# Kernel tuning notes

Measured on AMD Instinct MI355X. Metric: run time of the kernel, lower is better.

Reference implementation:

```python
import jax, jax.numpy as jnp
import numpy as np


def setup_inputs() -> dict:
    key = jax.random.key(0)
    k1, k2, k3, k4 = jax.random.split(key, 4)
    B, C, H, W = 2, 3, 160, 160
    n, L, s, k = 3000, 72, 4, 5
    return {
        "x": jax.random.normal(k1, (B, C, H, W), dtype=jnp.float32),
        "queries": jax.random.normal(k2, (B, L, H, W), dtype=jnp.float32),
        "keys": jax.random.normal(k3, (n, L), dtype=jnp.float32),
        "values": jax.random.normal(k4, (n, s * s, k * k), dtype=jnp.float32),
        "s": s,
        "k": k,
    }


def reference(x, queries, keys, values, s, k):
    B, C, H, W = x.shape
    pad = k // 2
    # reflect-pad spatial dims (matches F.pad mode='reflect')
    xp = jnp.pad(x, ((0, 0), (0, 0), (pad, pad), (pad, pad)), mode="reflect")
    # extract k*k patches: [B, C, H, W, k*k] (fixed small loop over k*k offsets)
    patches = jnp.stack(
        [xp[:, :, i : i + H, j : j + W] for i in range(k) for j in range(k)],
        axis=-1,
    )
    # per-pixel top-1 routing over codebook keys
    q = queries.transpose(0, 2, 3, 1)  # [B, H, W, L]
    sim = jnp.einsum("bhwl,nl->bhwn", q, keys)  # [B, H, W, n]
    idx = jnp.argmax(sim, axis=-1)  # [B, H, W] int
    v = values[idx]  # gather per-pixel kernel: [B, H, W, s^2, k^2]
    # per-pixel dynamic conv: [B, C, s^2, H, W]
    out = jnp.einsum("bchwk,bhwsk->bcshw", patches, v)
    # pixel shuffle with upscale s: [B, C, s^2, H, W] -> [B, C, H*s, W*s]
    out = out.reshape(B, C, s, s, H, W)
    out = out.transpose(0, 1, 4, 2, 5, 3)  # [B, C, H, s, W, s]
    return out.reshape(B, C, H * s, W * s)
```

## Files before the change

### kernel.cpp

```cpp
#include <hip/hip_runtime.h>

#define H 160
#define W 160
#define HW 25600
#define BB 2
#define CC 3
#define LL 72
#define NKEYS 3000
#define NT 94
#define NSPL 4
#define NPIX (BB * HW)

#define CERR 3e-5f
#define ABSG 1e-3f

typedef __attribute__((ext_vector_type(8))) short bf8v;
typedef __attribute__((ext_vector_type(16))) float f16v;

union FU { uint4 u4; bf8v v; };

#define WS_KFRAG 1024
#define WS_B1    963584
#define WS_B2    1782784
#define WS_BI    2601984
#define WS_THR   3421184
#define WS_LIST  3625984
#define WS_IDX   3830784

__device__ inline unsigned bf16rn(float f) {
    unsigned u = __float_as_uint(f);
    return (u + 0x7FFFu + ((u >> 16) & 1u)) >> 16;
}

__global__ __launch_bounds__(64) void kprep_kernel(
    const float* __restrict__ keys, unsigned* __restrict__ ctrl,
    uint4* __restrict__ kfg)
{
    const int tile = blockIdx.x;
    const int lane = threadIdx.x;
    const int key  = tile * 32 + (lane & 31);
    const int half = lane >> 5;
    const bool kv  = (key < NKEYS);
    float kmax = 0.f;
#pragma unroll
    for (int ks = 0; ks < 5; ++ks) {
        unsigned wh[4], wl[4];
#pragma unroll
        for (int j = 0; j < 4; ++j) {
            const int l0 = ks * 16 + half * 8 + 2 * j;
            float v0 = (kv && l0     < LL) ? keys[(size_t)key * LL + l0]     : 0.f;
            float v1 = (kv && l0 + 1 < LL) ? keys[(size_t)key * LL + l0 + 1] : 0.f;
            kmax = fmaxf(kmax, fmaxf(fabsf(v0), fabsf(v1)));
            unsigned h0 = bf16rn(v0), h1 = bf16rn(v1);
            float r0 = v0 - __uint_as_float(h0 << 16);
            float r1 = v1 - __uint_as_float(h1 << 16);
            wh[j] = h0 | (h1 << 16);
            wl[j] = bf16rn(r0) | (bf16rn(r1) << 16);
        }
        const int base = tile * 640 + (ks * 2) * 64 + lane;
        kfg[base]      = make_uint4(wh[0], wh[1], wh[2], wh[3]);
        kfg[base + 64] = make_uint4(wl[0], wl[1], wl[2], wl[3]);
    }
#pragma unroll
    for (int m = 32; m >= 1; m >>= 1)
        kmax = fmaxf(kmax, __shfl_xor(kmax, m));
    if (lane == 0) atomicMax(&ctrl[1], __float_as_uint(kmax));
}

__device__ __forceinline__ void build_qfrag(
    const float* __restrict__ qp, int hv, FU* qh, FU* ql, float& Ssum)
{
    Ssum = 0.f;
#pragma unroll
    for (int ks = 0; ks < 5; ++ks) {
        unsigned wh[4], wl[4];
#pragma unroll
        for (int j = 0; j < 4; ++j) {
            const int l0 = ks * 16 + hv * 8 + 2 * j;
            float v0 = (l0     < LL) ? qp[(size_t)l0 * HW]       : 0.f;
            float v1 = (l0 + 1 < LL) ? qp[(size_t)(l0 + 1) * HW] : 0.f;
            Ssum += fabsf(v0) + fabsf(v1);
            unsigned h0 = bf16rn(v0), h1 = bf16rn(v1);
            float r0 = v0 - __uint_as_float(h0 << 16);
            float r1 = v1 - __uint_as_float(h1 << 16);
            wh[j] = h0 | (h1 << 16);
            wl[j] = bf16rn(r0) | (bf16rn(r1) << 16);
        }
        qh[ks].u4 = make_uint4(wh[0], wh[1], wh[2], wh[3]);
        ql[ks].u4 = make_uint4(wl[0], wl[1], wl[2], wl[3]);
    }
}

template<bool LAST>
__device__ __forceinline__ void do_tile2(
    const uint4* __restrict__ kfg, int tileIdx,
    const FU* __restrict__ qhA, const FU* __restrict__ qlA,
    const FU* __restrict__ qhB, const FU* __restrict__ qlB,
    int lane, int hb,
    float& b1A, float& b2A, int& biA,
    float& b1B, float& b2B, int& biB)
{
    const uint4* __restrict__ kt = kfg + (size_t)tileIdx * 640;
    f16v accA, accB;
#pragma unroll
    for (int r = 0; r < 16; ++r) { accA[r] = 0.f; accB[r] = 0.f; }
#pragma unroll
    for (int ks = 0; ks < 5; ++ks) {
        FU kh, kl;
        kh.u4 = kt[ks * 128 + lane];
        kl.u4 = kt[ks * 128 + 64 + lane];
        accA = __builtin_amdgcn_mfma_f32_32x32x16_bf16(kh.v, qhA[ks].v, accA, 0, 0, 0);
        accB = __builtin_amdgcn_mfma_f32_32x32x16_bf16(kh.v, qhB[ks].v, accB, 0, 0, 0);
        accA = __builtin_amdgcn_mfma_f32_32x32x16_bf16(kh.v, qlA[ks].v, accA, 0, 0, 0);
        accB = __builtin_amdgcn_mfma_f32_32x32x16_bf16(kh.v, qlB[ks].v, accB, 0, 0, 0);
        accA = __builtin_amdgcn_mfma_f32_32x32x16_bf16(kl.v, qhA[ks].v, accA, 0, 0, 0);
        accB = __builtin_amdgcn_mfma_f32_32x32x16_bf16(kl.v, qhB[ks].v, accB, 0, 0, 0);
    }
    const int kb0 = tileIdx * 32 + hb;
    const int NR = LAST ? 12 : 16;
#pragma unroll
    for (int r = 0; r < NR; ++r) {
        const int key = kb0 + ((r & 3) + 8 * (r >> 2));
        {
            const float s = accA[r];
            const float n2 = __builtin_amdgcn_fmed3f(b1A, b2A, s);
            const bool gt = (s > b1A);
            b1A = fmaxf(b1A, s); b2A = n2; biA = gt ? key : biA;
        }
        {
            const float s = accB[r];
            const float n2 = __builtin_amdgcn_fmed3f(b1B, b2B, s);
            const bool gt = (s > b1B);
            b1B = fmaxf(b1B, s); b2B = n2; biB = gt ? key : biB;
        }
    }
}

__global__ __launch_bounds__(256) void route_kernel(
    const float* __restrict__ queries,
    const uint4* __restrict__ kfg,
    const unsigned* __restrict__ ctrl,
    float* __restrict__ b1s, float* __restrict__ b2s,
    int* __restrict__ bis, float* __restrict__ thr)
{
    const int tid   = threadIdx.x;
    const int lane  = tid & 63;
    const int wid   = tid >> 6;
    const int hv    = lane >> 5;
    const int hb    = 4 * hv;
    const int split = blockIdx.y;
    const int pA = blockIdx.x * 256 + wid * 64 + (lane & 31);
    const int pB = pA + 32;

    FU qhA[5], qlA[5], qhB[5], qlB[5];
    float SsA, SsB;
    {
        const int bA = pA / HW, hwA = pA - bA * HW;
        build_qfrag(queries + (size_t)bA * LL * HW + hwA, hv, qhA, qlA, SsA);
        const int bB = pB / HW, hwB = pB - bB * HW;
        build_qfrag(queries + (size_t)bB * LL * HW + hwB, hv, qhB, qlB, SsB);
    }

    float b1A = -3.0e38f, b2A = -3.0e38f; int biA = 0;
    float b1B = -3.0e38f, b2B = -3.0e38f; int biB = 0;

    const int t0 = split * 24;
    int tend = (split == NSPL - 1) ? NT : (t0 + 24);
    const bool haslast = (tend == NT);
    if (haslast) tend -= 1;

    for (int t = t0; t < tend; ++t)
        do_tile2<false>(kfg, t, qhA, qlA, qhB, qlB, lane, hb,
                        b1A, b2A, biA, b1B, b2B, biB);
    if (haslast)
        do_tile2<true >(kfg, NT - 1, qhA, qlA, qhB, qlB, lane, hb,
                        b1A, b2A, biA, b1B, b2B, biB);

    const float o1A = __shfl_xor(b1A, 32), o2A = __shfl_xor(b2A, 32);
    const int   oiA = __shfl_xor(biA, 32);
    const float n2A = fmaxf(fminf(b1A, o1A), fmaxf(b2A, o2A));
    const bool  tkA = (o1A > b1A) || (o1A == b1A && oiA < biA);
    const float n1A = fmaxf(b1A, o1A);
    const int   niA = tkA ? oiA : biA;

    const float o1B = __shfl_xor(b1B, 32), o2B = __shfl_xor(b2B, 32);
    const int   oiB = __shfl_xor(biB, 32);
    const float n2B = fmaxf(fminf(b1B, o1B), fmaxf(b2B, o2B));
    const bool  tkB = (o1B > b1B) || (o1B == b1B && oiB < biB);
    const float n1B = fmaxf(b1B, o1B);
    const int   niB = tkB ? oiB : biB;

    if ((lane & 32) == 0) {
        const int sp = split * NPIX;
        b1s[sp + pA] = n1A; b2s[sp + pA] = n2A; bis[sp + pA] = niA;
        b1s[sp + pB] = n1B; b2s[sp + pB] = n2B; bis[sp + pB] = niB;
        if (split == 0) {
            const float kmax = __uint_as_float(ctrl[1]);
            const float SpA = SsA + __shfl_xor(SsA, 32);
            const float SpB = SsB + __shfl_xor(SsB, 32);
            thr[pA] = 2.0f * (CERR * SpA * kmax + ABSG);
            thr[pB] = 2.0f * (CERR * SpB * kmax + ABSG);
        }
    }
}

__global__ __launch_bounds__(256) void combine_kernel(
    const float* __restrict__ b1s, const float* __restrict__ b2s,
    const int* __restrict__ bis, const float* __restrict__ thr,
    unsigned* __restrict__ ctrl, unsigned* __restrict__ list,
    int* __restrict__ idx_buf)
{
    const int p = blockIdx.x * 256 + threadIdx.x;
    float m1 = -3.0e38f, m2 = -3.0e38f; int bi = 0;
#pragma unroll
    for (int s = 0; s < NSPL; ++s) {
        const float a1 = b1s[s * NPIX + p];
        const float a2 = b2s[s * NPIX + p];
        const int   ai = bis[s * NPIX + p];
        if (a1 > m1) { m2 = fmaxf(m1, a2); m1 = a1; bi = ai; }
        else         { m2 = fmaxf(m2, a1); }
    }
    if ((m1 - m2) > thr[p]) idx_buf[p] = bi;
    else { unsigned pos = atomicAdd(&ctrl[0], 1u); list[pos] = (unsigned)p; }
}

__global__ __launch_bounds__(256) void cleanup_kernel(
    const float* __restrict__ queries, const float* __restrict__ keys,
    const unsigned* __restrict__ ctrl, const unsigned* __restrict__ list,
    int* __restrict__ idx_buf)
{
    __shared__ float qs[LL];
    __shared__ float rbest[4];
    __shared__ int   ridx[4];

    const int tid = threadIdx.x;
    const int ln  = tid & 63;
    const int wid = tid >> 6;
    const unsigned count = ctrl[0];

    for (unsigned u = blockIdx.x; u < count; u += gridDim.x) {
        const int p  = (int)list[u];
        const int b  = p / HW;
        const int hw = p - b * HW;

        __syncthreads();
        if (tid < LL)
            qs[tid] = queries[((size_t)b * LL + tid) * HW + hw];
        __syncthreads();

        float q[LL];
#pragma unroll
        for (int l = 0; l < LL; ++l) q[l] = qs[l];

        float best = -3.0e38f; int bidx = 0x7FFFFFFF;
#pragma unroll 1
        for (int it = 0; it < 12; ++it) {
            const int n  = it * 256 + tid;
            const int nc = (n < NKEYS) ? n : (NKEYS - 1);
            const float4* __restrict__ kr = (const float4*)(keys + (size_t)nc * LL);
            float a0 = 0.f, a1 = 0.f, a2 = 0.f, a3 = 0.f;
#pragma unroll
            for (int j = 0; j < 18; ++j) {
                float4 kv = kr[j];
                a0 = fmaf(q[4 * j + 0], kv.x, a0);
                a1 = fmaf(q[4 * j + 1], kv.y, a1);
                a2 = fmaf(q[4 * j + 2], kv.z, a2);
                a3 = fmaf(q[4 * j + 3], kv.w, a3);
            }
            const float s = (a0 + a1) + (a2 + a3);
            if (n < NKEYS && (s > best || (s == best && n < bidx))) { best = s; bidx = n; }
        }
#pragma unroll
        for (int m = 32; m >= 1; m >>= 1) {
            const float ob = __shfl_xor(best, m);
            const int   oi = __shfl_xor(bidx, m);
            if (ob > best || (ob == best && oi < bidx)) { best = ob; bidx = oi; }
        }
        if (ln == 0) { rbest[wid] = best; ridx[wid] = bidx; }
        __syncthreads();
        if (tid == 0) {
            float fb = rbest[0]; int fi = ridx[0];
#pragma unroll
            for (int wvi = 1; wvi < 4; ++wvi) {
                if (rbest[wvi] > fb || (rbest[wvi] == fb && ridx[wvi] < fi)) {
                    fb = rbest[wvi]; fi = ridx[wvi];
                }
            }
            idx_buf[p] = fi;
        }
    }
}

__global__ __launch_bounds__(256) void conv_kernel(
    const float* __restrict__ x,
    const float* __restrict__ values,
    const int* __restrict__ idx_buf,
    float* __restrict__ out)
{
    const int p  = blockIdx.x * 256 + threadIdx.x;
    const int b  = p / HW;
    const int hw = p - b * HW;
    const int h  = hw / W;
    const int w  = hw - h * W;

    const int idx = idx_buf[p];

    float patch[CC][25];
#pragma unroll
    for (int i = 0; i < 5; ++i) {
        int r = h + i - 2;
        r = (r < 0) ? -r : ((r >= H) ? (2 * H - 2 - r) : r);
#pragma unroll
        for (int j = 0; j < 5; ++j) {
            int cidx = w + j - 2;
            cidx = (cidx < 0) ? -cidx : ((cidx >= W) ? (2 * W - 2 - cidx) : cidx);
#pragma unroll
            for (int c = 0; c < CC; ++c)
                patch[c][i * 5 + j] = x[((size_t)(b * CC + c) * H + r) * W + cidx];
        }
    }

    const float* vbase = values + (size_t)idx * 400;
    float acc[CC][16];
#pragma unroll
    for (int c = 0; c < CC; ++c)
#pragma unroll
        for (int si = 0; si < 16; ++si) acc[c][si] = 0.f;

#pragma unroll
    for (int si = 0; si < 16; ++si) {
        float v[25];
#pragma unroll
        for (int kk = 0; kk < 25; ++kk) v[kk] = vbase[si * 25 + kk];
#pragma unroll
        for (int c = 0; c < CC; ++c) {
            float a = 0.f;
#pragma unroll
            for (int kk = 0; kk < 25; ++kk) a += patch[c][kk] * v[kk];
            acc[c][si] = a;
        }
    }

#pragma unroll
    for (int c = 0; c < CC; ++c) {
#pragma unroll
        for (int sy = 0; sy < 4; ++sy) {
            float4 o = make_float4(acc[c][sy * 4 + 0], acc[c][sy * 4 + 1],
                                   acc[c][sy * 4 + 2], acc[c][sy * 4 + 3]);
            size_t off = ((size_t)(b * CC + c) * (H * 4) + (h * 4 + sy)) * (size_t)(W * 4)
                         + (size_t)w * 4;
            *(float4*)(&out[off]) = o;
        }
    }
}

extern "C" void kernel_launch(void* const* d_in, const int* in_sizes, int n_in,
                              void* d_out, int out_size, void* d_ws, size_t ws_size,
                              hipStream_t stream) {
    const float* x       = (const float*)d_in[0];
    const float* queries = (const float*)d_in[1];
    const float* keys    = (const float*)d_in[2];
    const float* values  = (const float*)d_in[3];
    float* out = (float*)d_out;

    char* ws = (char*)d_ws;
    unsigned* ctrl = (unsigned*)ws;
    uint4*    kfg  = (uint4*)(ws + WS_KFRAG);
    float*    b1s  = (float*)(ws + WS_B1);
    float*    b2s  = (float*)(ws + WS_B2);
    int*      bis  = (int*)(ws + WS_BI);
    float*    thr  = (float*)(ws + WS_THR);
    unsigned* list = (unsigned*)(ws + WS_LIST);
    int*      idxb = (int*)(ws + WS_IDX);

    hipMemsetAsync(d_ws, 0, 8, stream);
    kprep_kernel<<<NT, 64, 0, stream>>>(keys, ctrl, kfg);
    route_kernel<<<dim3(NPIX / 256, NSPL), 256, 0, stream>>>(queries, kfg, ctrl,
                                                             b1s, b2s, bis, thr);
    combine_kernel<<<NPIX / 256, 256, 0, stream>>>(b1s, b2s, bis, thr, ctrl, list, idxb);
    cleanup_kernel<<<2048, 256, 0, stream>>>(queries, keys, ctrl, list, idxb);
    conv_kernel<<<NPIX / 256, 256, 0, stream>>>(x, values, idxb, out);
}
```

Baseline: 167.0 us.

## Stage key tiles in LDS and process two pixel groups per wave

The routing kernel now copies each split's key fragment tiles into shared memory in two halves and has each wave process two 64-pixel groups against them, with larger 512-thread blocks and a smaller grid. The goal is to cut repeated global/L2 reads of the key fragments by reusing them across more pixels per block. In exchange, query fragments are rebuilt for each half, doubling query loads, and the large LDS footprint plus a 200-block grid reduces occupancy and CU coverage.

```diff
diff --git a/kernel.cpp b/kernel.cpp
--- a/kernel.cpp
+++ b/kernel.cpp
@@ -92,23 +92,22 @@
 }
 
 template<bool LAST>
-__device__ __forceinline__ void do_tile2(
-    const uint4* __restrict__ kfg, int tileIdx,
+__device__ __forceinline__ void comp_tile_lds(
+    const uint4* __restrict__ kb, int tileIdx,
     const FU* __restrict__ qhA, const FU* __restrict__ qlA,
     const FU* __restrict__ qhB, const FU* __restrict__ qlB,
     int lane, int hb,
     float& b1A, float& b2A, int& biA,
     float& b1B, float& b2B, int& biB)
 {
-    const uint4* __restrict__ kt = kfg + (size_t)tileIdx * 640;
     f16v accA, accB;
 #pragma unroll
     for (int r = 0; r < 16; ++r) { accA[r] = 0.f; accB[r] = 0.f; }
 #pragma unroll
     for (int ks = 0; ks < 5; ++ks) {
         FU kh, kl;
-        kh.u4 = kt[ks * 128 + lane];
-        kl.u4 = kt[ks * 128 + 64 + lane];
+        kh.u4 = kb[ks * 128 + lane];
+        kl.u4 = kb[ks * 128 + 64 + lane];
         accA = __builtin_amdgcn_mfma_f32_32x32x16_bf16(kh.v, qhA[ks].v, accA, 0, 0, 0);
         accB = __builtin_amdgcn_mfma_f32_32x32x16_bf16(kh.v, qhB[ks].v, accB, 0, 0, 0);
         accA = __builtin_amdgcn_mfma_f32_32x32x16_bf16(kh.v, qlA[ks].v, accA, 0, 0, 0);
@@ -136,70 +135,114 @@
     }
 }
 
-__global__ __launch_bounds__(256) void route_kernel(
+__device__ __forceinline__ void run_round(
+    const uint4* __restrict__ kbuf, int gtile0, int hcount, bool haslast,
+    const float* __restrict__ queries, int pA, int hv, int hb, int lane,
+    float& b1A, float& b2A, int& biA,
+    float& b1B, float& b2B, int& biB,
+    float& SsA, float& SsB)
+{
+    const int pB = pA + 32;
+    FU qhA[5], qlA[5], qhB[5], qlB[5];
+    {
+        const int bA = pA / HW, hwA = pA - bA * HW;
+        build_qfrag(queries + (size_t)bA * LL * HW + hwA, hv, qhA, qlA, SsA);
+        const int bB = pB / HW, hwB = pB - bB * HW;
+        build_qfrag(queries + (size_t)bB * LL * HW + hwB, hv, qhB, qlB, SsB);
+    }
+    const int nmain = hcount - (haslast ? 1 : 0);
+#pragma unroll 1
+    for (int t = 0; t < nmain; ++t)
+        comp_tile_lds<false>(kbuf + t * 640, gtile0 + t, qhA, qlA, qhB, qlB,
+                             lane, hb, b1A, b2A, biA, b1B, b2B, biB);
+    if (haslast)
+        comp_tile_lds<true>(kbuf + (hcount - 1) * 640, gtile0 + hcount - 1,
+                            qhA, qlA, qhB, qlB, lane, hb,
+                            b1A, b2A, biA, b1B, b2B, biB);
+}
+
+__global__ __launch_bounds__(512, 2) void route_kernel(
     const float* __restrict__ queries,
     const uint4* __restrict__ kfg,
     const unsigned* __restrict__ ctrl,
     float* __restrict__ b1s, float* __restrict__ b2s,
     int* __restrict__ bis, float* __restrict__ thr)
 {
+    __shared__ uint4 kbuf[12 * 640];
+
     const int tid   = threadIdx.x;
     const int lane  = tid & 63;
     const int wid   = tid >> 6;
     const int hv    = lane >> 5;
     const int hb    = 4 * hv;
     const int split = blockIdx.y;
-    const int pA = blockIdx.x * 256 + wid * 64 + (lane & 31);
-    const int pB = pA + 32;
-
-    FU qhA[5], qlA[5], qhB[5], qlB[5];
-    float SsA, SsB;
-    {
-        const int bA = pA / HW, hwA = pA - bA * HW;
-        build_qfrag(queries + (size_t)bA * LL * HW + hwA, hv, qhA, qlA, SsA);
-        const int bB = pB / HW, hwB = pB - bB * HW;
-        build_qfrag(queries + (size_t)bB * LL * HW + hwB, hv, qhB, qlB, SsB);
-    }
-
-    float b1A = -3.0e38f, b2A = -3.0e38f; int biA = 0;
-    float b1B = -3.0e38f, b2B = -3.0e38f; int biB = 0;
-
-    const int t0 = split * 24;
-    int tend = (split == NSPL - 1) ? NT : (t0 + 24);
-    const bool haslast = (tend == NT);
-    if (haslast) tend -= 1;
-
-    for (int t = t0; t < tend; ++t)
-        do_tile2<false>(kfg, t, qhA, qlA, qhB, qlB, lane, hb,
-                        b1A, b2A, biA, b1B, b2B, biB);
-    if (haslast)
-        do_tile2<true >(kfg, NT - 1, qhA, qlA, qhB, qlB, lane, hb,
-                        b1A, b2A, biA, b1B, b2B, biB);
-
-    const float o1A = __shfl_xor(b1A, 32), o2A = __shfl_xor(b2A, 32);
-    const int   oiA = __shfl_xor(biA, 32);
-    const float n2A = fmaxf(fminf(b1A, o1A), fmaxf(b2A, o2A));
-    const bool  tkA = (o1A > b1A) || (o1A == b1A && oiA < biA);
-    const float n1A = fmaxf(b1A, o1A);
-    const int   niA = tkA ? oiA : biA;
-
-    const float o1B = __shfl_xor(b1B, 32), o2B = __shfl_xor(b2B, 32);
-    const int   oiB = __shfl_xor(biB, 32);
-    const float n2B = fmaxf(fminf(b1B, o1B), fmaxf(b2B, o2B));
-    const bool  tkB = (o1B > b1B) || (o1B == b1B && oiB < biB);
-    const float n1B = fmaxf(b1B, o1B);
-    const int   niB = tkB ? oiB : biB;
-
-    if ((lane & 32) == 0) {
-        const int sp = split * NPIX;
-        b1s[sp + pA] = n1A; b2s[sp + pA] = n2A; bis[sp + pA] = niA;
-        b1s[sp + pB] = n1B; b2s[sp + pB] = n2B; bis[sp + pB] = niB;
-        if (split == 0) {
-            const float kmax = __uint_as_float(ctrl[1]);
-            const float SpA = SsA + __shfl_xor(SsA, 32);
-            const float SpB = SsB + __shfl_xor(SsB, 32);
-            thr[pA] = 2.0f * (CERR * SpA * kmax + ABSG);
-            thr[pB] = 2.0f * (CERR * SpB * kmax + ABSG);
+
+    const int g0  = blockIdx.x * 16 + wid;
+    const int pA0 = g0 * 64 + (lane & 31);
+    const int pA1 = pA0 + 8 * 64;
+
+    const int t_begin = split * 24;
+    const int t_count = (split == NSPL - 1) ? (NT - 3 * 24) : 24;
+
+    float b1A0 = -3.0e38f, b2A0 = -3.0e38f, b1B0 = -3.0e38f, b2B0 = -3.0e38f;
+    float b1A1 = -3.0e38f, b2A1 = -3.0e38f, b1B1 = -3.0e38f, b2B1 = -3.0e38f;
+    int   biA0 = 0, biB0 = 0, biA1 = 0, biB1 = 0;
+    float SsA0 = 0.f, SsB0 = 0.f, SsA1 = 0.f, SsB1 = 0.f;
+
+#pragma unroll 1
+    for (int half = 0; half < 2; ++half) {
+        const int h0 = half * 12;
+        const int hcount = (t_count - h0 < 12) ? (t_count - h0) : 12;
+        const int stage_n = hcount * 640;
+
+        __syncthreads();
+#pragma unroll 2
+        for (int i = tid; i < stage_n; i += 512)
+            kbuf[i] = kfg[(size_t)(t_begin + h0) * 640 + i];
+        __syncthreads();
+
+        const bool haslast = (split == NSPL - 1) && (half == 1);
+        run_round(kbuf, t_begin + h0, hcount, haslast, queries, pA0, hv, hb, lane,
+                  b1A0, b2A0, biA0, b1B0, b2B0, biB0, SsA0, SsB0);
+        run_round(kbuf, t_begin + h0, hcount, haslast, queries, pA1, hv, hb, lane,
+                  b1A1, b2A1, biA1, b1B1, b2B1, biB1, SsA1, SsB1);
+    }
+
+    const float kmaxv = __uint_as_float(ctrl[1]);
+    const int sp = split * NPIX;
+
+#pragma unroll
+    for (int r = 0; r < 2; ++r) {
+        const float b1A = r ? b1A1 : b1A0, b2A = r ? b2A1 : b2A0;
+        const float b1B = r ? b1B1 : b1B0, b2B = r ? b2B1 : b2B0;
+        const int   biA = r ? biA1 : biA0, biB = r ? biB1 : biB0;
+        const float SsA = r ? SsA1 : SsA0, SsB = r ? SsB1 : SsB0;
+        const int   pA  = r ? pA1 : pA0;
+        const int   pB  = pA + 32;
+
+        const float o1A = __shfl_xor(b1A, 32), o2A = __shfl_xor(b2A, 32);
+        const int   oiA = __shfl_xor(biA, 32);
+        const float n2A = fmaxf(fminf(b1A, o1A), fmaxf(b2A, o2A));
+        const bool  tkA = (o1A > b1A) || (o1A == b1A && oiA < biA);
+        const float n1A = fmaxf(b1A, o1A);
+        const int   niA = tkA ? oiA : biA;
+
+        const float o1B = __shfl_xor(b1B, 32), o2B = __shfl_xor(b2B, 32);
+        const int   oiB = __shfl_xor(biB, 32);
+        const float n2B = fmaxf(fminf(b1B, o1B), fmaxf(b2B, o2B));
+        const bool  tkB = (o1B > b1B) || (o1B == b1B && oiB < biB);
+        const float n1B = fmaxf(b1B, o1B);
+        const int   niB = tkB ? oiB : biB;
+
+        if ((lane & 32) == 0) {
+            b1s[sp + pA] = n1A; b2s[sp + pA] = n2A; bis[sp + pA] = niA;
+            b1s[sp + pB] = n1B; b2s[sp + pB] = n2B; bis[sp + pB] = niB;
+            if (split == 0) {
+                const float SpA = SsA + __shfl_xor(SsA, 32);
+                const float SpB = SsB + __shfl_xor(SsB, 32);
+                thr[pA] = 2.0f * (CERR * SpA * kmaxv + ABSG);
+                thr[pB] = 2.0f * (CERR * SpB * kmaxv + ABSG);
+            }
         }
     }
 }
@@ -375,8 +418,8 @@
 
     hipMemsetAsync(d_ws, 0, 8, stream);
     kprep_kernel<<<NT, 64, 0, stream>>>(keys, ctrl, kfg);
-    route_kernel<<<dim3(NPIX / 256, NSPL), 256, 0, stream>>>(queries, kfg, ctrl,
-                                                             b1s, b2s, bis, thr);
+    route_kernel<<<dim3(50, NSPL), 512, 0, stream>>>(queries, kfg, ctrl,
+                                                     b1s, b2s, bis, thr);
     combine_kernel<<<NPIX / 256, 256, 0, stream>>>(b1s, b2s, bis, thr, ctrl, list, idxb);
     cleanup_kernel<<<2048, 256, 0, stream>>>(queries, keys, ctrl, list, idxb);
     conv_kernel<<<NPIX / 256, 256, 0, stream>>>(x, values, idxb, out);
```

New measurement: 169.1 us. About the same (+1.3%).

## Double-buffer key tiles in LDS via async global-to-LDS loads in routing kernel

Applied to the files above, without the earlier changes.

The routing kernel now stages each 32-key bf16 fragment tile into shared memory with global_load_lds, using two buffers so the next tile loads while the current one feeds the MFMAs. Before, every wave read the same key tile straight from global memory. The change is meant to cut redundant global/L2 traffic across the four waves and hide load latency. In exchange it adds two block-wide barriers per tile and LDS use, which can lower occupancy. Correctness depends on the wave-uniform LDS base pattern of global_load_lds lining up with the per-lane reads.

```diff
diff --git a/kernel.cpp b/kernel.cpp
--- a/kernel.cpp
+++ b/kernel.cpp
@@ -27,6 +27,9 @@
 #define WS_LIST  3625984
 #define WS_IDX   3830784
 
+#define GPTR(p) ((const __attribute__((address_space(1))) void*)(p))
+#define LPTR(p) ((__attribute__((address_space(3))) void*)(p))
+
 __device__ inline unsigned bf16rn(float f) {
     unsigned u = __float_as_uint(f);
     return (u + 0x7FFFu + ((u >> 16) & 1u)) >> 16;
@@ -91,24 +94,36 @@
     }
 }
 
+__device__ __forceinline__ void stage_tile(
+    const uint4* __restrict__ src, uint4* lbuf, int tid, int wid)
+{
+    __builtin_amdgcn_global_load_lds(GPTR(src + tid),
+                                     LPTR(lbuf + (tid & ~63)), 16, 0, 0);
+    __builtin_amdgcn_global_load_lds(GPTR(src + 256 + tid),
+                                     LPTR(lbuf + 256 + (tid & ~63)), 16, 0, 0);
+    if (wid < 2) {
+        __builtin_amdgcn_global_load_lds(GPTR(src + 512 + tid),
+                                         LPTR(lbuf + 512 + (tid & ~63)), 16, 0, 0);
+    }
+}
+
 template<bool LAST>
-__device__ __forceinline__ void do_tile2(
-    const uint4* __restrict__ kfg, int tileIdx,
+__device__ __forceinline__ void comp_tile_lds(
+    const uint4* __restrict__ kb, int tileIdx,
     const FU* __restrict__ qhA, const FU* __restrict__ qlA,
     const FU* __restrict__ qhB, const FU* __restrict__ qlB,
     int lane, int hb,
     float& b1A, float& b2A, int& biA,
     float& b1B, float& b2B, int& biB)
 {
-    const uint4* __restrict__ kt = kfg + (size_t)tileIdx * 640;
     f16v accA, accB;
 #pragma unroll
     for (int r = 0; r < 16; ++r) { accA[r] = 0.f; accB[r] = 0.f; }
 #pragma unroll
     for (int ks = 0; ks < 5; ++ks) {
         FU kh, kl;
-        kh.u4 = kt[ks * 128 + lane];
-        kl.u4 = kt[ks * 128 + 64 + lane];
+        kh.u4 = kb[ks * 128 + lane];
+        kl.u4 = kb[ks * 128 + 64 + lane];
         accA = __builtin_amdgcn_mfma_f32_32x32x16_bf16(kh.v, qhA[ks].v, accA, 0, 0, 0);
         accB = __builtin_amdgcn_mfma_f32_32x32x16_bf16(kh.v, qhB[ks].v, accB, 0, 0, 0);
         accA = __builtin_amdgcn_mfma_f32_32x32x16_bf16(kh.v, qlA[ks].v, accA, 0, 0, 0);
@@ -143,6 +158,8 @@
     float* __restrict__ b1s, float* __restrict__ b2s,
     int* __restrict__ bis, float* __restrict__ thr)
 {
+    __shared__ uint4 sbuf[2][640];
+
     const int tid   = threadIdx.x;
     const int lane  = tid & 63;
     const int wid   = tid >> 6;
@@ -164,17 +181,29 @@
     float b1A = -3.0e38f, b2A = -3.0e38f; int biA = 0;
     float b1B = -3.0e38f, b2B = -3.0e38f; int biB = 0;
 
-    const int t0 = split * 24;
-    int tend = (split == NSPL - 1) ? NT : (t0 + 24);
-    const bool haslast = (tend == NT);
-    if (haslast) tend -= 1;
-
-    for (int t = t0; t < tend; ++t)
-        do_tile2<false>(kfg, t, qhA, qlA, qhB, qlB, lane, hb,
-                        b1A, b2A, biA, b1B, b2B, biB);
-    if (haslast)
-        do_tile2<true >(kfg, NT - 1, qhA, qlA, qhB, qlB, lane, hb,
-                        b1A, b2A, biA, b1B, b2B, biB);
+    const int t0     = split * 24;
+    const int tcount = (split == NSPL - 1) ? (NT - 3 * 24) : 24;
+
+    stage_tile(kfg + (size_t)t0 * 640, sbuf[0], tid, wid);
+    __syncthreads();
+
+#pragma unroll 1
+    for (int i = 0; i < tcount; i += 2) {
+        stage_tile(kfg + (size_t)(t0 + i + 1) * 640, sbuf[1], tid, wid);
+        comp_tile_lds<false>(sbuf[0], t0 + i, qhA, qlA, qhB, qlB, lane, hb,
+                             b1A, b2A, biA, b1B, b2B, biB);
+        __syncthreads();
+
+        if (i + 2 < tcount)
+            stage_tile(kfg + (size_t)(t0 + i + 2) * 640, sbuf[0], tid, wid);
+        if (t0 + i + 1 == NT - 1)
+            comp_tile_lds<true >(sbuf[1], t0 + i + 1, qhA, qlA, qhB, qlB, lane, hb,
+                                 b1A, b2A, biA, b1B, b2B, biB);
+        else
+            comp_tile_lds<false>(sbuf[1], t0 + i + 1, qhA, qlA, qhB, qlB, lane, hb,
+                                 b1A, b2A, biA, b1B, b2B, biB);
+        __syncthreads();
+    }
 
     const float o1A = __shfl_xor(b1A, 32), o2A = __shfl_xor(b2A, 32);
     const int   oiA = __shfl_xor(biA, 32);
```

Measured after the change: 174.9 us. 4.7% more time.
